# Optimization experiments

Measured on AMD Instinct MI355X. Metric: run time of the kernel, lower is better.

## Reference

```python
import jax, jax.numpy as jnp
import numpy as np

D_MODEL = 1024
HEADS = 16
D_K = D_MODEL // HEADS
NEG_INF = -1e10


def setup_inputs() -> dict:
    key = jax.random.key(0)
    ks = jax.random.split(key, 10)
    n, s = 2, 2048
    inp = {
        "value": jax.random.normal(ks[0], (n, s, D_MODEL), dtype=jnp.float32),
        "key": jax.random.normal(ks[1], (n, s, D_MODEL), dtype=jnp.float32),
        "query": jax.random.normal(ks[2], (n, s, D_MODEL), dtype=jnp.float32),
        "mask": jax.random.randint(ks[3], (n, 1, s, s), 0, 2, dtype=jnp.int32),
        # torch.nn.Linear weights are [out, in]; y = x @ W.T (+ b)
        "Wq": jax.random.normal(ks[4], (D_MODEL, D_MODEL), dtype=jnp.float32) * (D_MODEL ** -0.5),
        "Wk": jax.random.normal(ks[5], (D_MODEL, D_MODEL), dtype=jnp.float32) * (D_MODEL ** -0.5),
        "Wv": jax.random.normal(ks[6], (D_MODEL, D_MODEL), dtype=jnp.float32) * (D_MODEL ** -0.5),
        "Wo": jax.random.normal(ks[7], (D_MODEL, D_MODEL), dtype=jnp.float32) * (D_MODEL ** -0.5),
        "bo": jax.random.normal(ks[8], (D_MODEL,), dtype=jnp.float32) * 0.01,
    }
    return inp


def reference(value, key, query, mask, Wq, Wk, Wv, Wo, bo):
    n, q_len, _ = query.shape
    # projections (Linear, no bias): x @ W.T
    q = (query @ Wq.T).reshape(n, q_len, HEADS, D_K)
    k = (key @ Wk.T).reshape(n, key.shape[1], HEADS, D_K)
    v = (value @ Wv.T).reshape(n, value.shape[1], HEADS, D_K)
    scores = jnp.einsum('nqhd,nkhd->nhqk', q, k)  # [n,h,q,k]
    scores = jnp.where(mask == 0, jnp.float32(NEG_INF), scores)
    attn = jax.nn.softmax(scores / jnp.sqrt(jnp.float32(D_K)), axis=-1)
    out = jnp.einsum('nhql,nlhd->nqhd', attn, v).reshape(n, q_len, D_MODEL)
    return out @ Wo.T + bo
```

## Files before the change

### kernel.cpp

```cpp
#include <hip/hip_runtime.h>
#include <hip/hip_bf16.h>
#include <stdint.h>

#define SEQ     2048
#define NBATCH  2
#define DMODEL  1024
#define NH      16
#define DKH     64

typedef __bf16 bf16;
typedef __attribute__((ext_vector_type(8))) __bf16 bf16x8;
typedef __attribute__((ext_vector_type(4))) __bf16 bf16x4;
typedef __attribute__((ext_vector_type(4))) float  f32x4;

static __device__ __forceinline__ f32x4 mfma16(bf16x8 a, bf16x8 b, f32x4 c) {
    return __builtin_amdgcn_mfma_f32_16x16x32_bf16(a, b, c, 0, 0, 0);
}

typedef const __attribute__((address_space(1))) void* gas_cptr;
typedef __attribute__((address_space(3))) void*       las_ptr;
#define GLDS16(g, l) __builtin_amdgcn_global_load_lds((gas_cptr)(g), (las_ptr)(l), 16, 0, 0)

#define PL32SWAP(a, b) asm("v_permlane32_swap_b32 %0, %1" : "+v"(a), "+v"(b))
#define PL16SWAP(a, b) asm("v_permlane16_swap_b32 %0, %1" : "+v"(a), "+v"(b))

__global__ __launch_bounds__(256) void cvt_all_k(const float* __restrict__ q,
                                                 const float* __restrict__ k,
                                                 const float* __restrict__ v,
                                                 const float* __restrict__ wq,
                                                 const float* __restrict__ wk,
                                                 const float* __restrict__ wv,
                                                 const float* __restrict__ wo,
                                                 const int* __restrict__ mask,
                                                 bf16* __restrict__ qb, bf16* __restrict__ kb,
                                                 bf16* __restrict__ vb, bf16* __restrict__ wqb,
                                                 bf16* __restrict__ wkb, bf16* __restrict__ wvb,
                                                 bf16* __restrict__ wob,
                                                 unsigned long long* __restrict__ mbits) {
    if (blockIdx.y == 7) {
        const int nwords = NBATCH * SEQ * (SEQ / 64);
        int wave  = (blockIdx.x * blockDim.x + threadIdx.x) >> 6;
        int lane  = threadIdx.x & 63;
        int nwtot = (gridDim.x * blockDim.x) >> 6;
        for (int w = wave; w < nwords; w += nwtot) {
            int m = mask[(size_t)w * 64 + lane];
            unsigned long long b = __ballot(m != 0);
            if (lane == 0) mbits[w] = b;
        }
        return;
    }
    const float* src; bf16* dst; int n4;
    const int NX4 = (NBATCH * SEQ * DMODEL) / 4, NW4 = (DMODEL * DMODEL) / 4;
    switch (blockIdx.y) {
        case 0: src = q;  dst = qb;  n4 = NX4; break;
        case 1: src = k;  dst = kb;  n4 = NX4; break;
        case 2: src = v;  dst = vb;  n4 = NX4; break;
        case 3: src = wq; dst = wqb; n4 = NW4; break;
        case 4: src = wk; dst = wkb; n4 = NW4; break;
        case 5: src = wv; dst = wvb; n4 = NW4; break;
        default: src = wo; dst = wob; n4 = NW4; break;
    }
    int stride = gridDim.x * blockDim.x;
    for (int i = blockIdx.x * blockDim.x + threadIdx.x; i < n4; i += stride) {
        f32x4 f = ((const f32x4*)src)[i];
        bf16x4 o;
#pragma unroll
        for (int j = 0; j < 4; j++) o[j] = (bf16)f[j];
        ((bf16x4*)dst)[i] = o;
    }
}

__global__ __launch_bounds__(256) void qkv_gemm(const bf16* __restrict__ Xq,
                                                const bf16* __restrict__ Xk,
                                                const bf16* __restrict__ Xv,
                                                const bf16* __restrict__ Wq,
                                                const bf16* __restrict__ Wk,
                                                const bf16* __restrict__ Wv,
                                                bf16* __restrict__ Qo,
                                                bf16* __restrict__ Ko,
                                                bf16* __restrict__ Vto) {
    __shared__ bf16 As[128 * 32], Bs[128 * 32];
    const int z = blockIdx.z;
    const bf16* A = (z == 0) ? Xq : (z == 1) ? Xk : Xv;
    const bf16* W = (z == 0) ? Wq : (z == 1) ? Wk : Wv;
    const int bm = blockIdx.x * 128, bn = blockIdx.y * 128;
    const int tid = threadIdx.x, wave = tid >> 6, lane = tid & 63;
    const int wm = wave >> 1, wn = wave & 1, lo = lane & 15, hi = lane >> 4;

    const int r0 = wave * 32 + (lane >> 2);
    const int c8 = (lane & 3) * 8;
    const bf16* Ag = A + (size_t)(bm + r0) * DMODEL + c8;
    const bf16* Bg = W + (size_t)(bn + r0) * DMODEL + c8;
    bf16* lA = &As[wave * 1024];
    bf16* lB = &Bs[wave * 1024];

    f32x4 acc[4][4];
#pragma unroll
    for (int i = 0; i < 4; i++)
#pragma unroll
        for (int j = 0; j < 4; j++) acc[i][j] = 0.0f;

    for (int k0 = 0; k0 < DMODEL; k0 += 32) {
        __syncthreads();
        GLDS16(Ag + k0, lA);
        GLDS16(Ag + k0 + (size_t)16 * DMODEL, lA + 512);
        GLDS16(Bg + k0, lB);
        GLDS16(Bg + k0 + (size_t)16 * DMODEL, lB + 512);
        __syncthreads();

        bf16x8 a[4], b[4];
#pragma unroll
        for (int t = 0; t < 4; t++) {
            a[t] = *(const bf16x8*)&As[(wm * 64 + t * 16 + lo) * 32 + hi * 8];
            b[t] = *(const bf16x8*)&Bs[(wn * 64 + t * 16 + lo) * 32 + hi * 8];
        }
        if (z < 2) {
#pragma unroll
            for (int tm = 0; tm < 4; tm++)
#pragma unroll
                for (int tn = 0; tn < 4; tn++)
                    acc[tm][tn] = mfma16(a[tm], b[tn], acc[tm][tn]);
        } else {
#pragma unroll
            for (int tm = 0; tm < 4; tm++)
#pragma unroll
                for (int tn = 0; tn < 4; tn++)
                    acc[tm][tn] = mfma16(b[tn], a[tm], acc[tm][tn]);
        }
    }

    if (z < 2) {
        bf16* O = (z == 0) ? Qo : Ko;
        const float qscale = (z == 0) ? 0.18033688f : 1.0f;
#pragma unroll
        for (int tm = 0; tm < 4; tm++)
#pragma unroll
            for (int tn = 0; tn < 4; tn++)
#pragma unroll
                for (int r = 0; r < 4; r++) {
                    int m = bm + wm * 64 + tm * 16 + hi * 4 + r;
                    int o = bn + wn * 64 + tn * 16 + lo;
                    int nidx = m >> 11, sq = m & 2047;
                    int hh = o >> 6, d = o & 63;
                    O[(((size_t)nidx * NH + hh) * SEQ + sq) * DKH + d] = (bf16)(acc[tm][tn][r] * qscale);
                }
    } else {
#pragma unroll
        for (int tm = 0; tm < 4; tm++)
#pragma unroll
            for (int tn = 0; tn < 4; tn++)
#pragma unroll
                for (int r = 0; r < 4; r++) {
                    int o = bn + wn * 64 + tn * 16 + hi * 4 + r;
                    int m = bm + wm * 64 + tm * 16 + lo;
                    int nidx = m >> 11, sq = m & 2047;
                    int hh = o >> 6, d = o & 63;
                    Vto[(((size_t)nidx * NH + hh) * DKH + d) * SEQ + sq] = (bf16)acc[tm][tn][r];
                }
    }
}

__global__ __launch_bounds__(256, 4) void attn_k(const bf16* __restrict__ Q,
                                                 const bf16* __restrict__ K,
                                                 const bf16* __restrict__ Vt,
                                                 const unsigned long long* __restrict__ mbits,
                                                 bf16* __restrict__ Op0,
                                                 bf16* __restrict__ Op1,
                                                 bf16* __restrict__ Op2,
                                                 bf16* __restrict__ Op3,
                                                 float* __restrict__ Lp,
                                                 int ksrange) {
    __shared__ bf16 Ks[64 * 72];
    __shared__ bf16 Vs[64 * 72];

    const int bid = blockIdx.x;
    const int xcd = bid & 7, j = bid >> 3;
    const int hd = xcd * 4 + (j & 3);
    const int qb = (j >> 2) & 15;
    const int ks = j >> 6;
    const int n = hd >> 4, h = hd & 15;

    const int tid = threadIdx.x, wave = tid >> 6, lane = tid & 63;
    const int lo = lane & 15, hi = lane >> 4;

    const size_t headoff = (size_t)hd * SEQ * DKH;
    const bf16* Qh = Q + headoff;
    const bf16* Kh = K + headoff;
    const bf16* Vh = Vt + headoff;

    const int qrowA = qb * 128 + wave * 16 + lo;
    const int qrowB = qrowA + 64;
    const bf16x8 aq0A = *(const bf16x8*)(Qh + (size_t)qrowA * DKH + hi * 8);
    const bf16x8 aq1A = *(const bf16x8*)(Qh + (size_t)qrowA * DKH + 32 + hi * 8);
    const bf16x8 aq0B = *(const bf16x8*)(Qh + (size_t)qrowB * DKH + hi * 8);
    const bf16x8 aq1B = *(const bf16x8*)(Qh + (size_t)qrowB * DKH + 32 + hi * 8);

    bf16x8 ones;
#pragma unroll
    for (int i = 0; i < 8; i++) ones[i] = (bf16)1.0f;

    f32x4 oaccA[4], oaccB[4];
#pragma unroll
    for (int t = 0; t < 4; t++) { oaccA[t] = 0.0f; oaccB[t] = 0.0f; }
    f32x4 laccA; laccA = 0.0f;
    f32x4 laccB; laccB = 0.0f;

    const unsigned long long* mbqA = mbits + ((size_t)n * SEQ + qrowA) * (SEQ / 64);
    const unsigned long long* mbqB = mbits + ((size_t)n * SEQ + qrowB) * (SEQ / 64);

    const int kbeg = ks * ksrange, kend = kbeg + ksrange;

    const int srow = tid >> 3, sseg = tid & 7;
    const bf16* Kg = Kh + (size_t)srow * DKH + sseg * 8;
    const bf16* Vg = Vh + (size_t)srow * SEQ + sseg * 8;

    bf16x8 rk0 = *(const bf16x8*)(Kg + (size_t)kbeg * DKH);
    bf16x8 rk1 = *(const bf16x8*)(Kg + (size_t)(kbeg + 32) * DKH);
    bf16x8 rv0 = *(const bf16x8*)(Vg + kbeg);
    bf16x8 rv1 = *(const bf16x8*)(Vg + (size_t)32 * SEQ + kbeg);
    unsigned long long wmA = mbqA[kbeg >> 6];
    unsigned long long wmB = mbqB[kbeg >> 6];
    unsigned long long wmnA = 0, wmnB = 0;

    union FragU { uint32_t u[4]; bf16x8 v; };

#pragma unroll 1
    for (int k0 = kbeg; k0 < kend; k0 += 64) {
        __syncthreads();
        *(bf16x8*)&Ks[srow * 72 + sseg * 8]        = rk0;
        *(bf16x8*)&Ks[(srow + 32) * 72 + sseg * 8] = rk1;
        *(bf16x8*)&Vs[srow * 72 + sseg * 8]        = rv0;
        *(bf16x8*)&Vs[(srow + 32) * 72 + sseg * 8] = rv1;
        if (k0 + 64 < kend) {
            rk0 = *(const bf16x8*)(Kg + (size_t)(k0 + 64) * DKH);
            rk1 = *(const bf16x8*)(Kg + (size_t)(k0 + 96) * DKH);
            rv0 = *(const bf16x8*)(Vg + k0 + 64);
            rv1 = *(const bf16x8*)(Vg + (size_t)32 * SEQ + k0 + 64);
            wmnA = mbqA[(k0 >> 6) + 1];
            wmnB = mbqB[(k0 >> 6) + 1];
        }
        __syncthreads();

        unsigned wloA = (unsigned)(wmA >> (hi * 4));
        unsigned whiA = (unsigned)(wmA >> (hi * 4 + 32));
        unsigned wloB = (unsigned)(wmB >> (hi * 4));
        unsigned whiB = (unsigned)(wmB >> (hi * 4 + 32));
        uint32_t pkA[4][2], pkB[4][2];
#pragma unroll
        for (int tn = 0; tn < 4; tn++) {
            const int kr = (tn * 16 + lo) * 72;
            bf16x8 b0 = *(const bf16x8*)&Ks[kr + hi * 8];
            bf16x8 b1 = *(const bf16x8*)&Ks[kr + 32 + hi * 8];
            f32x4 zA; zA = 0.0f;
            zA = mfma16(b0, aq0A, zA);
            zA = mfma16(b1, aq1A, zA);
            f32x4 zB; zB = 0.0f;
            zB = mfma16(b0, aq0B, zB);
            zB = mfma16(b1, aq1B, zB);
            unsigned wsA = ((tn < 2) ? wloA : whiA) >> ((tn & 1) * 16);
            unsigned wsB = ((tn < 2) ? wloB : whiB) >> ((tn & 1) * 16);
            float pvA[4], pvB[4];
#pragma unroll
            for (int r = 0; r < 4; r++) {
                float eA = __builtin_amdgcn_exp2f(zA[r]);
                pvA[r] = ((wsA >> r) & 1u) ? eA : 0.0f;
                float eB = __builtin_amdgcn_exp2f(zB[r]);
                pvB[r] = ((wsB >> r) & 1u) ? eB : 0.0f;
            }
            asm("v_cvt_pk_bf16_f32 %0, %1, %2" : "=v"(pkA[tn][0]) : "v"(pvA[0]), "v"(pvA[1]));
            asm("v_cvt_pk_bf16_f32 %0, %1, %2" : "=v"(pkA[tn][1]) : "v"(pvA[2]), "v"(pvA[3]));
            asm("v_cvt_pk_bf16_f32 %0, %1, %2" : "=v"(pkB[tn][0]) : "v"(pvB[0]), "v"(pvB[1]));
            asm("v_cvt_pk_bf16_f32 %0, %1, %2" : "=v"(pkB[tn][1]) : "v"(pvB[2]), "v"(pvB[3]));
        }
        wmA = wmnA;
        wmB = wmnB;

        bf16x8 ap0A, ap1A, ap0B, ap1B;
        {
            uint32_t d00 = pkA[0][0], d02 = pkA[1][0];
            PL32SWAP(d00, d02); PL16SWAP(d00, d02);
            uint32_t d01 = pkA[0][1], d03 = pkA[1][1];
            PL32SWAP(d01, d03); PL16SWAP(d01, d03);
            uint32_t d10 = pkA[2][0], d12 = pkA[3][0];
            PL32SWAP(d10, d12); PL16SWAP(d10, d12);
            uint32_t d11 = pkA[2][1], d13 = pkA[3][1];
            PL32SWAP(d11, d13); PL16SWAP(d11, d13);
            FragU f0, f1;
            f0.u[0] = d00; f0.u[1] = d01; f0.u[2] = d02; f0.u[3] = d03;
            f1.u[0] = d10; f1.u[1] = d11; f1.u[2] = d12; f1.u[3] = d13;
            ap0A = f0.v; ap1A = f1.v;
        }
        {
            uint32_t d00 = pkB[0][0], d02 = pkB[1][0];
            PL32SWAP(d00, d02); PL16SWAP(d00, d02);
            uint32_t d01 = pkB[0][1], d03 = pkB[1][1];
            PL32SWAP(d01, d03); PL16SWAP(d01, d03);
            uint32_t d10 = pkB[2][0], d12 = pkB[3][0];
            PL32SWAP(d10, d12); PL16SWAP(d10, d12);
            uint32_t d11 = pkB[2][1], d13 = pkB[3][1];
            PL32SWAP(d11, d13); PL16SWAP(d11, d13);
            FragU f0, f1;
            f0.u[0] = d00; f0.u[1] = d01; f0.u[2] = d02; f0.u[3] = d03;
            f1.u[0] = d10; f1.u[1] = d11; f1.u[2] = d12; f1.u[3] = d13;
            ap0B = f0.v; ap1B = f1.v;
        }

#pragma unroll
        for (int td = 0; td < 4; td++) {
            bf16x8 b0 = *(const bf16x8*)&Vs[(td * 16 + lo) * 72 + hi * 8];
            bf16x8 b1 = *(const bf16x8*)&Vs[(td * 16 + lo) * 72 + 32 + hi * 8];
            oaccA[td] = mfma16(ap0A, b0, oaccA[td]);
            oaccA[td] = mfma16(ap1A, b1, oaccA[td]);
            oaccB[td] = mfma16(ap0B, b0, oaccB[td]);
            oaccB[td] = mfma16(ap1B, b1, oaccB[td]);
        }
        laccA = mfma16(ap0A, ones, laccA);
        laccA = mfma16(ap1A, ones, laccA);
        laccB = mfma16(ap0B, ones, laccB);
        laccB = mfma16(ap1B, ones, laccB);
    }

    bf16* Op = (ks & 2) ? ((ks & 1) ? Op3 : Op2) : ((ks & 1) ? Op1 : Op0);
#pragma unroll
    for (int td = 0; td < 4; td++)
#pragma unroll
        for (int r = 0; r < 4; r++) {
            int qA = qb * 128 + wave * 16 + hi * 4 + r;
            int qB = qA + 64;
            int d = td * 16 + lo;
            Op[((size_t)n * SEQ + qA) * DMODEL + h * 64 + d] = (bf16)oaccA[td][r];
            Op[((size_t)n * SEQ + qB) * DMODEL + h * 64 + d] = (bf16)oaccB[td][r];
        }
    if (lo == 0) {
#pragma unroll
        for (int r = 0; r < 4; r++) {
            int qA = qb * 128 + wave * 16 + hi * 4 + r;
            int qB = qA + 64;
            size_t base = (size_t)ks * (NBATCH * NH * SEQ) + ((size_t)(n * NH + h) * SEQ);
            Lp[base + qA] = laccA[r];
            Lp[base + qB] = laccB[r];
        }
    }
}

__global__ __launch_bounds__(256) void merge_k(const bf16* o0, const bf16* o1,
                                               const bf16* o2, const bf16* o3,
                                               const float* lp, bf16* Aout,
                                               int nsplit) {
    int t = blockIdx.x * blockDim.x + threadIdx.x;
    int q = t >> 7;
    int h = (t >> 3) & 15;
    int n = q >> 11;
    const int NL = NBATCH * NH * SEQ;
    int li = (n * NH + h) * SEQ + (q & 2047);
    bf16x8 a = ((const bf16x8*)o0)[t];
    bf16x8 b = ((const bf16x8*)o1)[t];
    float l = lp[li] + lp[NL + li];
    float s[8];
#pragma unroll
    for (int i = 0; i < 8; i++) s[i] = (float)a[i] + (float)b[i];
    if (nsplit == 4) {
        bf16x8 c = ((const bf16x8*)o2)[t];
        bf16x8 d = ((const bf16x8*)o3)[t];
        l += lp[2 * NL + li] + lp[3 * NL + li];
#pragma unroll
        for (int i = 0; i < 8; i++) s[i] += (float)c[i] + (float)d[i];
    }
    float rl = 1.0f / l;
    bf16x8 o;
#pragma unroll
    for (int i = 0; i < 8; i++) o[i] = (bf16)(s[i] * rl);
    ((bf16x8*)Aout)[t] = o;
}

__global__ __launch_bounds__(256) void out_gemm(const bf16* __restrict__ A,
                                                const bf16* __restrict__ W,
                                                const float* __restrict__ bias,
                                                float* __restrict__ Out) {
    __shared__ bf16 As[128 * 32], Bs[128 * 32];
    const int bm = blockIdx.x * 128, bn = blockIdx.y * 128;
    const int tid = threadIdx.x, wave = tid >> 6, lane = tid & 63;
    const int wm = wave >> 1, wn = wave & 1, lo = lane & 15, hi = lane >> 4;

    const int r0 = wave * 32 + (lane >> 2);
    const int c8 = (lane & 3) * 8;
    const bf16* Ag = A + (size_t)(bm + r0) * DMODEL + c8;
    const bf16* Bg = W + (size_t)(bn + r0) * DMODEL + c8;
    bf16* lA = &As[wave * 1024];
    bf16* lB = &Bs[wave * 1024];

    f32x4 acc[4][4];
#pragma unroll
    for (int i = 0; i < 4; i++)
#pragma unroll
        for (int j = 0; j < 4; j++) acc[i][j] = 0.0f;

    for (int k0 = 0; k0 < DMODEL; k0 += 32) {
        __syncthreads();
        GLDS16(Ag + k0, lA);
        GLDS16(Ag + k0 + (size_t)16 * DMODEL, lA + 512);
        GLDS16(Bg + k0, lB);
        GLDS16(Bg + k0 + (size_t)16 * DMODEL, lB + 512);
        __syncthreads();

        bf16x8 a[4], b[4];
#pragma unroll
        for (int t = 0; t < 4; t++) {
            a[t] = *(const bf16x8*)&As[(wm * 64 + t * 16 + lo) * 32 + hi * 8];
            b[t] = *(const bf16x8*)&Bs[(wn * 64 + t * 16 + lo) * 32 + hi * 8];
        }
#pragma unroll
        for (int tm = 0; tm < 4; tm++)
#pragma unroll
            for (int tn = 0; tn < 4; tn++)
                acc[tm][tn] = mfma16(a[tm], b[tn], acc[tm][tn]);
    }

#pragma unroll
    for (int tm = 0; tm < 4; tm++)
#pragma unroll
        for (int tn = 0; tn < 4; tn++) {
            int o = bn + wn * 64 + tn * 16 + lo;
            float bv = bias[o];
#pragma unroll
            for (int r = 0; r < 4; r++) {
                int m = bm + wm * 64 + tm * 16 + hi * 4 + r;
                Out[(size_t)m * DMODEL + o] = acc[tm][tn][r] + bv;
            }
        }
}

extern "C" void kernel_launch(void* const* d_in, const int* in_sizes, int n_in,
                              void* d_out, int out_size, void* d_ws, size_t ws_size,
                              hipStream_t stream) {
    const float* value = (const float*)d_in[0];
    const float* key   = (const float*)d_in[1];
    const float* query = (const float*)d_in[2];
    const int*   mask  = (const int*)d_in[3];
    const float* Wq    = (const float*)d_in[4];
    const float* Wk    = (const float*)d_in[5];
    const float* Wv    = (const float*)d_in[6];
    const float* Wo    = (const float*)d_in[7];
    const float* bo    = (const float*)d_in[8];
    float* out = (float*)d_out;

    char* ws = (char*)d_ws;
    bf16* Qws = (bf16*)(ws);
    bf16* Kws = (bf16*)(ws + (8u  << 20));
    bf16* Vt  = (bf16*)(ws + (16u << 20));
    bf16* Xqb = (bf16*)(ws + (24u << 20));
    bf16* Xkb = (bf16*)(ws + (32u << 20));
    bf16* Xvb = (bf16*)(ws + (40u << 20));
    bf16* Wqb = (bf16*)(ws + (48u << 20));
    bf16* Wkb = (bf16*)(ws + (50u << 20));
    bf16* Wvb = (bf16*)(ws + (52u << 20));
    bf16* Wob = (bf16*)(ws + (54u << 20));
    unsigned long long* mbits = (unsigned long long*)(ws + (56u << 20));
    bf16*  Op0 = Xqb;
    bf16*  Op1 = Xkb;
    bf16*  Op2 = Xvb;
    bf16*  Op3 = Xvb;
    bf16*  Aws = Xqb;
    float* Lp  = (float*)Wqb;

    const int  ksn     = 2;
    const int  ksrange = SEQ / ksn;
    const int  attn_grid = 32 * 16 * ksn;

    cvt_all_k<<<dim3(1024, 8), 256, 0, stream>>>(query, key, value, Wq, Wk, Wv, Wo, mask,
                                                 Xqb, Xkb, Xvb, Wqb, Wkb, Wvb, Wob, mbits);
    qkv_gemm<<<dim3(32, 8, 3), 256, 0, stream>>>(Xqb, Xkb, Xvb, Wqb, Wkb, Wvb, Qws, Kws, Vt);
    attn_k<<<attn_grid, 256, 0, stream>>>(Qws, Kws, Vt, mbits, Op0, Op1, Op2, Op3, Lp, ksrange);
    merge_k<<<2048, 256, 0, stream>>>(Op0, Op1, Op2, Op3, Lp, Aws, ksn);
    out_gemm<<<dim3(32, 8), 256, 0, stream>>>(Aws, Wob, bo, out);
}
```

Before: 274.7 us.

## Double-buffer LDS tiles in QKV and output projection GEMMs

Both projection GEMMs now keep two LDS buffers. Each iteration issues the async global-to-LDS loads for the next K-slice before running the MFMAs on the current one, and uses one barrier per iteration instead of two. The aim is to hide global load latency behind compute and cut synchronisation. In exchange, LDS use doubles, which may lower occupancy, and it relies on the barrier to make the async loads visible.

Measured after the change: 278.6 us. Within noise of the previous version (+1.4%).

```diff
diff --git a/kernel.cpp b/kernel.cpp
--- a/kernel.cpp
+++ b/kernel.cpp
@@ -79,7 +79,7 @@
                                                 bf16* __restrict__ Qo,
                                                 bf16* __restrict__ Ko,
                                                 bf16* __restrict__ Vto) {
-    __shared__ bf16 As[128 * 32], Bs[128 * 32];
+    __shared__ bf16 As[2][128 * 32], Bs[2][128 * 32];
     const int z = blockIdx.z;
     const bf16* A = (z == 0) ? Xq : (z == 1) ? Xk : Xv;
     const bf16* W = (z == 0) ? Wq : (z == 1) ? Wk : Wv;
@@ -91,8 +91,7 @@
     const int c8 = (lane & 3) * 8;
     const bf16* Ag = A + (size_t)(bm + r0) * DMODEL + c8;
     const bf16* Bg = W + (size_t)(bn + r0) * DMODEL + c8;
-    bf16* lA = &As[wave * 1024];
-    bf16* lB = &Bs[wave * 1024];
+    const int woff = wave * 1024;
 
     f32x4 acc[4][4];
 #pragma unroll
@@ -100,19 +99,26 @@
 #pragma unroll
         for (int j = 0; j < 4; j++) acc[i][j] = 0.0f;
 
+    GLDS16(Ag, &As[0][woff]);
+    GLDS16(Ag + (size_t)16 * DMODEL, &As[0][woff + 512]);
+    GLDS16(Bg, &Bs[0][woff]);
+    GLDS16(Bg + (size_t)16 * DMODEL, &Bs[0][woff + 512]);
+    __syncthreads();
+
     for (int k0 = 0; k0 < DMODEL; k0 += 32) {
-        __syncthreads();
-        GLDS16(Ag + k0, lA);
-        GLDS16(Ag + k0 + (size_t)16 * DMODEL, lA + 512);
-        GLDS16(Bg + k0, lB);
-        GLDS16(Bg + k0 + (size_t)16 * DMODEL, lB + 512);
-        __syncthreads();
+        const int cur = (k0 >> 5) & 1;
+        if (k0 + 32 < DMODEL) {
+            GLDS16(Ag + k0 + 32, &As[cur ^ 1][woff]);
+            GLDS16(Ag + k0 + 32 + (size_t)16 * DMODEL, &As[cur ^ 1][woff + 512]);
+            GLDS16(Bg + k0 + 32, &Bs[cur ^ 1][woff]);
+            GLDS16(Bg + k0 + 32 + (size_t)16 * DMODEL, &Bs[cur ^ 1][woff + 512]);
+        }
 
         bf16x8 a[4], b[4];
 #pragma unroll
         for (int t = 0; t < 4; t++) {
-            a[t] = *(const bf16x8*)&As[(wm * 64 + t * 16 + lo) * 32 + hi * 8];
-            b[t] = *(const bf16x8*)&Bs[(wn * 64 + t * 16 + lo) * 32 + hi * 8];
+            a[t] = *(const bf16x8*)&As[cur][(wm * 64 + t * 16 + lo) * 32 + hi * 8];
+            b[t] = *(const bf16x8*)&Bs[cur][(wn * 64 + t * 16 + lo) * 32 + hi * 8];
         }
         if (z < 2) {
 #pragma unroll
@@ -127,6 +133,7 @@
                 for (int tn = 0; tn < 4; tn++)
                     acc[tm][tn] = mfma16(b[tn], a[tm], acc[tm][tn]);
         }
+        __syncthreads();
     }
 
     if (z < 2) {
@@ -377,7 +384,7 @@
                                                 const bf16* __restrict__ W,
                                                 const float* __restrict__ bias,
                                                 float* __restrict__ Out) {
-    __shared__ bf16 As[128 * 32], Bs[128 * 32];
+    __shared__ bf16 As[2][128 * 32], Bs[2][128 * 32];
     const int bm = blockIdx.x * 128, bn = blockIdx.y * 128;
     const int tid = threadIdx.x, wave = tid >> 6, lane = tid & 63;
     const int wm = wave >> 1, wn = wave & 1, lo = lane & 15, hi = lane >> 4;
@@ -386,8 +393,7 @@
     const int c8 = (lane & 3) * 8;
     const bf16* Ag = A + (size_t)(bm + r0) * DMODEL + c8;
     const bf16* Bg = W + (size_t)(bn + r0) * DMODEL + c8;
-    bf16* lA = &As[wave * 1024];
-    bf16* lB = &Bs[wave * 1024];
+    const int woff = wave * 1024;
 
     f32x4 acc[4][4];
 #pragma unroll
@@ -395,25 +401,33 @@
 #pragma unroll
         for (int j = 0; j < 4; j++) acc[i][j] = 0.0f;
 
+    GLDS16(Ag, &As[0][woff]);
+    GLDS16(Ag + (size_t)16 * DMODEL, &As[0][woff + 512]);
+    GLDS16(Bg, &Bs[0][woff]);
+    GLDS16(Bg + (size_t)16 * DMODEL, &Bs[0][woff + 512]);
+    __syncthreads();
+
     for (int k0 = 0; k0 < DMODEL; k0 += 32) {
-        __syncthreads();
-        GLDS16(Ag + k0, lA);
-        GLDS16(Ag + k0 + (size_t)16 * DMODEL, lA + 512);
-        GLDS16(Bg + k0, lB);
-        GLDS16(Bg + k0 + (size_t)16 * DMODEL, lB + 512);
-        __syncthreads();
+        const int cur = (k0 >> 5) & 1;
+        if (k0 + 32 < DMODEL) {
+            GLDS16(Ag + k0 + 32, &As[cur ^ 1][woff]);
+            GLDS16(Ag + k0 + 32 + (size_t)16 * DMODEL, &As[cur ^ 1][woff + 512]);
+            GLDS16(Bg + k0 + 32, &Bs[cur ^ 1][woff]);
+            GLDS16(Bg + k0 + 32 + (size_t)16 * DMODEL, &Bs[cur ^ 1][woff + 512]);
+        }
 
         bf16x8 a[4], b[4];
 #pragma unroll
         for (int t = 0; t < 4; t++) {
-            a[t] = *(const bf16x8*)&As[(wm * 64 + t * 16 + lo) * 32 + hi * 8];
-            b[t] = *(const bf16x8*)&Bs[(wn * 64 + t * 16 + lo) * 32 + hi * 8];
+            a[t] = *(const bf16x8*)&As[cur][(wm * 64 + t * 16 + lo) * 32 + hi * 8];
+            b[t] = *(const bf16x8*)&Bs[cur][(wn * 64 + t * 16 + lo) * 32 + hi * 8];
         }
 #pragma unroll
         for (int tm = 0; tm < 4; tm++)
 #pragma unroll
             for (int tn = 0; tn < 4; tn++)
                 acc[tm][tn] = mfma16(a[tm], b[tn], acc[tm][tn]);
+        __syncthreads();
     }
 
 #pragma unroll
```

## Fuse split-K merge into output GEMM and register-prefetch GEMM operands

Applied to the files above, without the earlier changes.

Removes the separate merge kernel: the output projection GEMM now reads both split-K partial outputs and their row sums, combines and normalizes them while staging A tiles into shared memory. Both GEMMs drop direct global-to-LDS loads in favor of register prefetch of the next K tile, overlapping global loads with compute. This saves one launch and a full intermediate write and read, but adds conversion arithmetic and extra global loads inside the GEMM's main loop, plus the loss of async LDS loads.

New measurement: 273.6 us. About the same (-0.4%).

```diff
diff --git a/kernel.cpp b/kernel.cpp
--- a/kernel.cpp
+++ b/kernel.cpp
@@ -16,10 +16,6 @@
 static __device__ __forceinline__ f32x4 mfma16(bf16x8 a, bf16x8 b, f32x4 c) {
     return __builtin_amdgcn_mfma_f32_16x16x32_bf16(a, b, c, 0, 0, 0);
 }
-
-typedef const __attribute__((address_space(1))) void* gas_cptr;
-typedef __attribute__((address_space(3))) void*       las_ptr;
-#define GLDS16(g, l) __builtin_amdgcn_global_load_lds((gas_cptr)(g), (las_ptr)(l), 16, 0, 0)
 
 #define PL32SWAP(a, b) asm("v_permlane32_swap_b32 %0, %1" : "+v"(a), "+v"(b))
 #define PL16SWAP(a, b) asm("v_permlane16_swap_b32 %0, %1" : "+v"(a), "+v"(b))
@@ -91,8 +87,8 @@
     const int c8 = (lane & 3) * 8;
     const bf16* Ag = A + (size_t)(bm + r0) * DMODEL + c8;
     const bf16* Bg = W + (size_t)(bn + r0) * DMODEL + c8;
-    bf16* lA = &As[wave * 1024];
-    bf16* lB = &Bs[wave * 1024];
+    bf16* lA = &As[wave * 1024 + (lane >> 2) * 32 + (lane & 3) * 8];
+    bf16* lB = &Bs[wave * 1024 + (lane >> 2) * 32 + (lane & 3) * 8];
 
     f32x4 acc[4][4];
 #pragma unroll
@@ -100,12 +96,24 @@
 #pragma unroll
         for (int j = 0; j < 4; j++) acc[i][j] = 0.0f;
 
+    bf16x8 ra0 = *(const bf16x8*)(Ag);
+    bf16x8 ra1 = *(const bf16x8*)(Ag + (size_t)16 * DMODEL);
+    bf16x8 rb0 = *(const bf16x8*)(Bg);
+    bf16x8 rb1 = *(const bf16x8*)(Bg + (size_t)16 * DMODEL);
+
+#pragma unroll 1
     for (int k0 = 0; k0 < DMODEL; k0 += 32) {
         __syncthreads();
-        GLDS16(Ag + k0, lA);
-        GLDS16(Ag + k0 + (size_t)16 * DMODEL, lA + 512);
-        GLDS16(Bg + k0, lB);
-        GLDS16(Bg + k0 + (size_t)16 * DMODEL, lB + 512);
+        *(bf16x8*)lA         = ra0;
+        *(bf16x8*)(lA + 512) = ra1;
+        *(bf16x8*)lB         = rb0;
+        *(bf16x8*)(lB + 512) = rb1;
+        if (k0 + 32 < DMODEL) {
+            ra0 = *(const bf16x8*)(Ag + k0 + 32);
+            ra1 = *(const bf16x8*)(Ag + k0 + 32 + (size_t)16 * DMODEL);
+            rb0 = *(const bf16x8*)(Bg + k0 + 32);
+            rb1 = *(const bf16x8*)(Bg + k0 + 32 + (size_t)16 * DMODEL);
+        }
         __syncthreads();
 
         bf16x8 a[4], b[4];
@@ -166,8 +174,6 @@
                                                  const unsigned long long* __restrict__ mbits,
                                                  bf16* __restrict__ Op0,
                                                  bf16* __restrict__ Op1,
-                                                 bf16* __restrict__ Op2,
-                                                 bf16* __restrict__ Op3,
                                                  float* __restrict__ Lp,
                                                  int ksrange) {
     __shared__ bf16 Ks[64 * 72];
@@ -320,7 +326,7 @@
         laccB = mfma16(ap1B, ones, laccB);
     }
 
-    bf16* Op = (ks & 2) ? ((ks & 1) ? Op3 : Op2) : ((ks & 1) ? Op1 : Op0);
+    bf16* Op = ks ? Op1 : Op0;
 #pragma unroll
     for (int td = 0; td < 4; td++)
 #pragma unroll
@@ -343,37 +349,9 @@
     }
 }
 
-__global__ __launch_bounds__(256) void merge_k(const bf16* o0, const bf16* o1,
-                                               const bf16* o2, const bf16* o3,
-                                               const float* lp, bf16* Aout,
-                                               int nsplit) {
-    int t = blockIdx.x * blockDim.x + threadIdx.x;
-    int q = t >> 7;
-    int h = (t >> 3) & 15;
-    int n = q >> 11;
-    const int NL = NBATCH * NH * SEQ;
-    int li = (n * NH + h) * SEQ + (q & 2047);
-    bf16x8 a = ((const bf16x8*)o0)[t];
-    bf16x8 b = ((const bf16x8*)o1)[t];
-    float l = lp[li] + lp[NL + li];
-    float s[8];
-#pragma unroll
-    for (int i = 0; i < 8; i++) s[i] = (float)a[i] + (float)b[i];
-    if (nsplit == 4) {
-        bf16x8 c = ((const bf16x8*)o2)[t];
-        bf16x8 d = ((const bf16x8*)o3)[t];
-        l += lp[2 * NL + li] + lp[3 * NL + li];
-#pragma unroll
-        for (int i = 0; i < 8; i++) s[i] += (float)c[i] + (float)d[i];
-    }
-    float rl = 1.0f / l;
-    bf16x8 o;
-#pragma unroll
-    for (int i = 0; i < 8; i++) o[i] = (bf16)(s[i] * rl);
-    ((bf16x8*)Aout)[t] = o;
-}
-
-__global__ __launch_bounds__(256) void out_gemm(const bf16* __restrict__ A,
+__global__ __launch_bounds__(256) void out_gemm(const bf16* __restrict__ o0,
+                                                const bf16* __restrict__ o1,
+                                                const float* __restrict__ lp,
                                                 const bf16* __restrict__ W,
                                                 const float* __restrict__ bias,
                                                 float* __restrict__ Out) {
@@ -384,10 +362,15 @@
 
     const int r0 = wave * 32 + (lane >> 2);
     const int c8 = (lane & 3) * 8;
-    const bf16* Ag = A + (size_t)(bm + r0) * DMODEL + c8;
+    const int m1 = bm + r0, m2 = m1 + 16;
+    const size_t aoff1 = (size_t)m1 * DMODEL + c8;
+    const size_t aoff2 = (size_t)m2 * DMODEL + c8;
     const bf16* Bg = W + (size_t)(bn + r0) * DMODEL + c8;
-    bf16* lA = &As[wave * 1024];
-    bf16* lB = &Bs[wave * 1024];
+    const int NL = NBATCH * NH * SEQ;
+    const int li1b = (m1 >> 11) * (NH * SEQ) + (m1 & 2047);
+    const int li2b = (m2 >> 11) * (NH * SEQ) + (m2 & 2047);
+    bf16* lA = &As[wave * 1024 + (lane >> 2) * 32 + (lane & 3) * 8];
+    bf16* lB = &Bs[wave * 1024 + (lane >> 2) * 32 + (lane & 3) * 8];
 
     f32x4 acc[4][4];
 #pragma unroll
@@ -395,12 +378,42 @@
 #pragma unroll
         for (int j = 0; j < 4; j++) acc[i][j] = 0.0f;
 
+    bf16x8 px0 = *(const bf16x8*)(o0 + aoff1);
+    bf16x8 py0 = *(const bf16x8*)(o1 + aoff1);
+    bf16x8 px1 = *(const bf16x8*)(o0 + aoff2);
+    bf16x8 py1 = *(const bf16x8*)(o1 + aoff2);
+    bf16x8 pb0 = *(const bf16x8*)(Bg);
+    bf16x8 pb1 = *(const bf16x8*)(Bg + (size_t)16 * DMODEL);
+    float pl1a = lp[li1b], pl1b = lp[NL + li1b];
+    float pl2a = lp[li2b], pl2b = lp[NL + li2b];
+
+#pragma unroll 1
     for (int k0 = 0; k0 < DMODEL; k0 += 32) {
         __syncthreads();
-        GLDS16(Ag + k0, lA);
-        GLDS16(Ag + k0 + (size_t)16 * DMODEL, lA + 512);
-        GLDS16(Bg + k0, lB);
-        GLDS16(Bg + k0 + (size_t)16 * DMODEL, lB + 512);
+        float rl1 = 1.0f / (pl1a + pl1b);
+        float rl2 = 1.0f / (pl2a + pl2b);
+        bf16x8 wa0, wa1;
+#pragma unroll
+        for (int jj = 0; jj < 8; jj++) {
+            wa0[jj] = (bf16)(((float)px0[jj] + (float)py0[jj]) * rl1);
+            wa1[jj] = (bf16)(((float)px1[jj] + (float)py1[jj]) * rl2);
+        }
+        *(bf16x8*)lA         = wa0;
+        *(bf16x8*)(lA + 512) = wa1;
+        *(bf16x8*)lB         = pb0;
+        *(bf16x8*)(lB + 512) = pb1;
+        if (k0 + 32 < DMODEL) {
+            int h = (k0 + 32) >> 6;
+            px0 = *(const bf16x8*)(o0 + aoff1 + k0 + 32);
+            py0 = *(const bf16x8*)(o1 + aoff1 + k0 + 32);
+            px1 = *(const bf16x8*)(o0 + aoff2 + k0 + 32);
+            py1 = *(const bf16x8*)(o1 + aoff2 + k0 + 32);
+            pb0 = *(const bf16x8*)(Bg + k0 + 32);
+            pb1 = *(const bf16x8*)(Bg + k0 + 32 + (size_t)16 * DMODEL);
+            int li1 = li1b + h * SEQ, li2 = li2b + h * SEQ;
+            pl1a = lp[li1]; pl1b = lp[NL + li1];
+            pl2a = lp[li2]; pl2b = lp[NL + li2];
+        }
         __syncthreads();
 
         bf16x8 a[4], b[4];
@@ -458,9 +471,6 @@
     unsigned long long* mbits = (unsigned long long*)(ws + (56u << 20));
     bf16*  Op0 = Xqb;
     bf16*  Op1 = Xkb;
-    bf16*  Op2 = Xvb;
-    bf16*  Op3 = Xvb;
-    bf16*  Aws = Xqb;
     float* Lp  = (float*)Wqb;
 
     const int  ksn     = 2;
@@ -470,7 +480,6 @@
     cvt_all_k<<<dim3(1024, 8), 256, 0, stream>>>(query, key, value, Wq, Wk, Wv, Wo, mask,
                                                  Xqb, Xkb, Xvb, Wqb, Wkb, Wvb, Wob, mbits);
     qkv_gemm<<<dim3(32, 8, 3), 256, 0, stream>>>(Xqb, Xkb, Xvb, Wqb, Wkb, Wvb, Qws, Kws, Vt);
-    attn_k<<<attn_grid, 256, 0, stream>>>(Qws, Kws, Vt, mbits, Op0, Op1, Op2, Op3, Lp, ksrange);
-    merge_k<<<2048, 256, 0, stream>>>(Op0, Op1, Op2, Op3, Lp, Aws, ksn);
-    out_gemm<<<dim3(32, 8), 256, 0, stream>>>(Aws, Wob, bo, out);
-}
+    attn_k<<<attn_grid, 256, 0, stream>>>(Qws, Kws, Vt, mbits, Op0, Op1, Lp, ksrange);
+    out_gemm<<<dim3(32, 8), 256, 0, stream>>>(Op0, Op1, Lp, Wob, bo, out);
+}
```
